# Kernel optimization log

Measured on AMD Instinct MI355X. Metric: run time of the kernel, lower is better.

## Reference

```python
import jax, jax.numpy as jnp
import numpy as np
import math

WINDOW = 257
W = (WINDOW - 1) // 2      # 128
Q_CH = WINDOW + 1          # 258 (query chunk size / stride)
K_CH = WINDOW * 2          # 514 (key window size)


def compl_mod(m, n):
    return int(n * math.ceil(m / n) - m)


def setup_inputs() -> dict:
    key = jax.random.key(0)
    k1, k2, k3 = jax.random.split(key, 3)
    b, s, nh, h = 2, 4096, 16, 64
    q = jax.random.normal(k1, (b, s, nh, h), jnp.float32)
    k = jax.random.normal(k2, (b, s, nh, h), jnp.float32)
    v = jax.random.normal(k3, (b, s, nh, h), jnp.float32)
    return {"q": q, "k": k, "v": v}


def reference(q, k, v):
    b, s, nh, h = q.shape
    q = q * h ** (-0.5)
    q_pad = compl_mod(s, Q_CH)
    k_pad = compl_mod(s + 2 * W - K_CH, Q_CH)
    c = (s + q_pad) // Q_CH  # number of chunks

    # pad along sequence dim (q right-padded; k/v haloed by w on both sides)
    qp = jnp.pad(q, ((0, 0), (0, q_pad), (0, 0), (0, 0)))
    kp = jnp.pad(k, ((0, 0), (W, W + k_pad), (0, 0), (0, 0)))
    vp = jnp.pad(v, ((0, 0), (W, W + k_pad), (0, 0), (0, 0)))

    # unfold: q non-overlapping chunks, k/v overlapping windows (size K_CH, stride Q_CH)
    qw = qp.reshape(b, c, Q_CH, nh, h)                              # [b,c,q,nh,h]
    idx = (jnp.arange(c) * Q_CH)[:, None] + jnp.arange(K_CH)[None]  # [c,K_CH]
    kw = kp[:, idx]                                                 # [b,c,k,nh,h]
    vw = vp[:, idx]

    A = jnp.einsum('bcqnh,bcknh->bncqk', qw, kw)  # [b,nh,c,Q_CH,K_CH]

    # banded mask: valid iff i <= j <= i + 2w (True = masked)
    i = jnp.arange(Q_CH)[:, None]
    j = jnp.arange(K_CH)[None, :]
    base = ~((j >= i) & (j <= i + 2 * W))
    mask_left = base.at[:, :W].set(True)                    # first chunk: no left halo
    mask_right = base.at[:, K_CH - (W + k_pad):].set(True)  # last chunk: no right halo/pad
    if c > 1:
        mask = jnp.concatenate(
            [mask_left[None], jnp.broadcast_to(base, (c - 2, Q_CH, K_CH)), mask_right[None]], axis=0)
    else:
        mask = (mask_left | mask_right)[None]

    mask_value = -jnp.finfo(A.dtype).max
    A = jnp.where(mask[None, None], mask_value, A)
    A = jax.nn.softmax(A, axis=-1)  # dropout omitted (eval mode)

    z = jnp.einsum('bncqk,bcknh->bncqh', A, vw)       # [b,nh,c,Q_CH,h]
    z = z.reshape(b, nh, c * Q_CH, h)[:, :, :s]       # trim q padding
    return jnp.transpose(z, (0, 2, 1, 3))             # [b,s,nh,h]
```

## Files before the change

### kernel.cpp

```cpp
#include <hip/hip_runtime.h>

typedef _Float16 h16;
typedef __attribute__((ext_vector_type(2))) _Float16 f16x2;
typedef __attribute__((ext_vector_type(4))) _Float16 f16x4;
typedef __attribute__((ext_vector_type(2))) __fp16   fp16x2n;
typedef __attribute__((ext_vector_type(8))) _Float16 f16x8;
typedef __attribute__((ext_vector_type(4))) float f32x4;

#define S_LEN 4096
#define NHEAD 16
#define HDIM  64
#define WIN   128
#define TQ    128
#define NCHT  12
#define KSTR  72
#define VSTR2 40
#define SSTR  40
#define QSCALE 0.18033688011112042f

static __device__ __forceinline__ f16x2 pk(float a, float b) {
    fp16x2n r = __builtin_amdgcn_cvt_pkrtz(a, b);
    return __builtin_bit_cast(f16x2, r);
}

static __device__ __forceinline__ f16x8 cvt8(float4 a, float4 b) {
    f16x2 p0 = pk(a.x, a.y), p1 = pk(a.z, a.w);
    f16x2 p2 = pk(b.x, b.y), p3 = pk(b.z, b.w);
    f16x8 r;
    r[0]=p0[0]; r[1]=p0[1]; r[2]=p1[0]; r[3]=p1[1];
    r[4]=p2[0]; r[5]=p2[1]; r[6]=p3[0]; r[7]=p3[1];
    return r;
}

__global__ __launch_bounds__(512, 4)
void wattn(const float* __restrict__ Qg, const float* __restrict__ Kg,
           const float* __restrict__ Vg, float* __restrict__ Og)
{
    __shared__ h16 Kbuf[3][32 * KSTR];
    __shared__ h16 Vbuf[3][64 * VSTR2];
    __shared__ h16 Slds[8 * 16 * SSTR];

    const int tid  = threadIdx.x;
    const int wid  = tid >> 6;
    const int lane = tid & 63;
    const int l15  = lane & 15;
    const int quad = lane >> 4;

    const int q0    = blockIdx.x * TQ;
    const int head  = blockIdx.y;
    const int b     = blockIdx.z;
    const int kbase = q0 - WIN;
    const int rowstride = NHEAD * HDIM;

    const float* KB = Kg + ((long)b * S_LEN * NHEAD + head) * HDIM;
    const float* VB = Vg + ((long)b * S_LEN * NHEAD + head) * HDIM;

    const int srow = tid >> 4;
    const int sh0  = (tid & 15) * 4;

    float4 kreg, vreg;
    #define SLOAD(i) do {                                                    \
        int kg_ = kbase + (i)*32 + srow;                                     \
        kg_ = kg_ < 0 ? 0 : (kg_ > S_LEN-1 ? S_LEN-1 : kg_);                 \
        const float* kp_ = KB + (long)kg_ * rowstride + sh0;                 \
        const float* vp_ = VB + (long)kg_ * rowstride + sh0;                 \
        kreg = *(const float4*)kp_;                                          \
        vreg = *(const float4*)vp_;                                          \
    } while (0)
    #define SWRITE(i) do {                                                   \
        int bi_ = (i) % 3;                                                   \
        f16x2 ka_ = pk(kreg.x, kreg.y), kb_ = pk(kreg.z, kreg.w);            \
        f16x4 kv_; kv_[0]=ka_[0]; kv_[1]=ka_[1]; kv_[2]=kb_[0]; kv_[3]=kb_[1];\
        *(f16x4*)&Kbuf[bi_][srow * KSTR + sh0] = kv_;                        \
        Vbuf[bi_][(sh0+0) * VSTR2 + srow] = (h16)vreg.x;                     \
        Vbuf[bi_][(sh0+1) * VSTR2 + srow] = (h16)vreg.y;                     \
        Vbuf[bi_][(sh0+2) * VSTR2 + srow] = (h16)vreg.z;                     \
        Vbuf[bi_][(sh0+3) * VSTR2 + srow] = (h16)vreg.w;                     \
    } while (0)

    SLOAD(0);

    f16x8 aQ0, aQ1;
    {
        const int qrow = q0 + wid * 16 + l15;
        const float* qp = Qg + ((long)(b * S_LEN + qrow) * NHEAD + head) * HDIM;
        float4 x0 = *(const float4*)(qp + quad*8);
        float4 x1 = *(const float4*)(qp + quad*8 + 4);
        float4 x2 = *(const float4*)(qp + 32 + quad*8);
        float4 x3 = *(const float4*)(qp + 32 + quad*8 + 4);
        x0.x*=QSCALE; x0.y*=QSCALE; x0.z*=QSCALE; x0.w*=QSCALE;
        x1.x*=QSCALE; x1.y*=QSCALE; x1.z*=QSCALE; x1.w*=QSCALE;
        x2.x*=QSCALE; x2.y*=QSCALE; x2.z*=QSCALE; x2.w*=QSCALE;
        x3.x*=QSCALE; x3.y*=QSCALE; x3.z*=QSCALE; x3.w*=QSCALE;
        aQ0 = cvt8(x0, x1);
        aQ1 = cvt8(x2, x3);
    }

    SWRITE(0);
    __syncthreads();

    int lo[4], hi[4];
    #pragma unroll
    for (int r = 0; r < 4; ++r) {
        int qg = q0 + wid*16 + quad*4 + r;
        lo[r] = (qg - WIN < 0) ? 0 : qg - WIN;
        hi[r] = (qg + WIN > S_LEN-1) ? S_LEN-1 : qg + WIN;
    }

    float l_r[4] = {0.f, 0.f, 0.f, 0.f};
    f32x4 Oacc[4];
    #pragma unroll
    for (int t = 0; t < 4; ++t) Oacc[t] = (f32x4){0.f,0.f,0.f,0.f};

    const int c0 = wid >> 1;
    h16* Sw = &Slds[wid * 16 * SSTR];

    for (int i = 0; i < NCHT; ++i) {
        if (i + 1 < NCHT) SLOAD(i + 1);

        if ((unsigned)(i - c0) < 9u) {
            const h16* Kb = Kbuf[i % 3];
            const h16* Vb = Vbuf[i % 3];

            f16x8 bK00 = *(const f16x8*)&Kb[ l15      * KSTR + quad*8];
            f16x8 bK01 = *(const f16x8*)&Kb[ l15      * KSTR + 32 + quad*8];
            f16x8 bK10 = *(const f16x8*)&Kb[(16+l15)  * KSTR + quad*8];
            f16x8 bK11 = *(const f16x8*)&Kb[(16+l15)  * KSTR + 32 + quad*8];

            f32x4 s0 = (f32x4){0.f,0.f,0.f,0.f};
            s0 = __builtin_amdgcn_mfma_f32_16x16x32_f16(aQ0, bK00, s0, 0, 0, 0);
            s0 = __builtin_amdgcn_mfma_f32_16x16x32_f16(aQ1, bK01, s0, 0, 0, 0);
            f32x4 s1 = (f32x4){0.f,0.f,0.f,0.f};
            s1 = __builtin_amdgcn_mfma_f32_16x16x32_f16(aQ0, bK10, s1, 0, 0, 0);
            s1 = __builtin_amdgcn_mfma_f32_16x16x32_f16(aQ1, bK11, s1, 0, 0, 0);

            const int col0 = kbase + i*32 + l15;
            const int col1 = col0 + 16;
            #pragma unroll
            for (int r = 0; r < 4; ++r) {
                float v0 = (col0 >= lo[r] && col0 <= hi[r]) ? s0[r] : -1e30f;
                float v1 = (col1 >= lo[r] && col1 <= hi[r]) ? s1[r] : -1e30f;
                float p0 = exp2f(v0);
                float p1 = exp2f(v1);
                l_r[r] += p0 + p1;
                Sw[(quad*4 + r) * SSTR + l15]      = (h16)p0;
                Sw[(quad*4 + r) * SSTR + 16 + l15] = (h16)p1;
            }

            __builtin_amdgcn_wave_barrier();

            f16x8 aP = *(const f16x8*)&Sw[l15 * SSTR + quad * 8];
            #pragma unroll
            for (int t = 0; t < 4; ++t) {
                f16x8 bV = *(const f16x8*)&Vb[(t*16 + l15) * VSTR2 + quad*8];
                Oacc[t] = __builtin_amdgcn_mfma_f32_16x16x32_f16(aP, bV, Oacc[t], 0, 0, 0);
            }
            __builtin_amdgcn_wave_barrier();
        }

        if (i + 1 < NCHT) SWRITE(i + 1);
        __syncthreads();
    }
    #undef SLOAD
    #undef SWRITE

    float* op = Og + ((long)(b * S_LEN + q0 + wid*16) * NHEAD + head) * HDIM;
    #pragma unroll
    for (int r = 0; r < 4; ++r) {
        float l = l_r[r];
        l += __shfl_xor(l, 1);
        l += __shfl_xor(l, 2);
        l += __shfl_xor(l, 4);
        l += __shfl_xor(l, 8);
        float inv = 1.0f / l;
        #pragma unroll
        for (int t = 0; t < 4; ++t) {
            op[(quad*4 + r) * rowstride + t*16 + l15] = Oacc[t][r] * inv;
        }
    }
}

extern "C" void kernel_launch(void* const* d_in, const int* in_sizes, int n_in,
                              void* d_out, int out_size, void* d_ws, size_t ws_size,
                              hipStream_t stream) {
    const float* q = (const float*)d_in[0];
    const float* k = (const float*)d_in[1];
    const float* v = (const float*)d_in[2];
    float* out = (float*)d_out;
    const int batch = in_sizes[0] / (S_LEN * NHEAD * HDIM);
    dim3 grid(S_LEN / TQ, NHEAD, batch);
    wattn<<<grid, 512, 0, stream>>>(q, k, v, out);
}
```

Before: 155.1 us.

## Double query tile to 256 with 16 waves, split K/V staging, swizzle LDS and blocks

Each block now covers 256 queries with 1024 threads (16 waves), so each staged K/V window is shared by twice as many queries and halo reloads drop. Staging is split: half the threads load K and half load V, one float4 each. XOR swizzles on the transposed V writes and on the P scratch reads and writes are meant to cut LDS bank conflicts. A block-index swizzle remaps workgroups across XCDs for L2 locality. The cost is a block barrier across 16 waves per chunk, and the 4-blocks-per-CU occupancy hint becomes 8 with 1024 threads, which is unlikely to be met.

```diff
diff --git a/kernel.cpp b/kernel.cpp
--- a/kernel.cpp
+++ b/kernel.cpp
@@ -11,8 +11,9 @@
 #define NHEAD 16
 #define HDIM  64
 #define WIN   128
-#define TQ    128
-#define NCHT  12
+#define TQ    256
+#define NQT   (S_LEN / TQ)
+#define NCHT  16
 #define KSTR  72
 #define VSTR2 40
 #define SSTR  40
@@ -32,13 +33,13 @@
     return r;
 }
 
-__global__ __launch_bounds__(512, 4)
+__global__ __launch_bounds__(1024, 8)
 void wattn(const float* __restrict__ Qg, const float* __restrict__ Kg,
            const float* __restrict__ Vg, float* __restrict__ Og)
 {
     __shared__ h16 Kbuf[3][32 * KSTR];
     __shared__ h16 Vbuf[3][64 * VSTR2];
-    __shared__ h16 Slds[8 * 16 * SSTR];
+    __shared__ h16 Slds[16 * 16 * SSTR];
 
     const int tid  = threadIdx.x;
     const int wid  = tid >> 6;
@@ -46,36 +47,45 @@
     const int l15  = lane & 15;
     const int quad = lane >> 4;
 
-    const int q0    = blockIdx.x * TQ;
-    const int head  = blockIdx.y;
-    const int b     = blockIdx.z;
+    int lin = blockIdx.x + NQT * (blockIdx.y + NHEAD * blockIdx.z);
+    int nwg = NQT * NHEAD * gridDim.z;
+    int swz = ((nwg & 7) == 0) ? ((lin & 7) * (nwg >> 3) + (lin >> 3)) : lin;
+    const int bx   = swz & (NQT - 1);
+    const int head = (swz / NQT) & (NHEAD - 1);
+    const int b    = swz / (NQT * NHEAD);
+
+    const int q0    = bx * TQ;
     const int kbase = q0 - WIN;
     const int rowstride = NHEAD * HDIM;
 
     const float* KB = Kg + ((long)b * S_LEN * NHEAD + head) * HDIM;
     const float* VB = Vg + ((long)b * S_LEN * NHEAD + head) * HDIM;
 
-    const int srow = tid >> 4;
-    const int sh0  = (tid & 15) * 4;
-
-    float4 kreg, vreg;
+    const bool isK = (tid < 512);
+    const int srow = (tid >> 4) & 31;
+    const int ish  = tid & 15;
+    const int sh0  = ish * 4;
+    const int vkey = ((srow + (((ish >> 2) & 3) << 3)) & 31) ^ ((ish & 3) << 3);
+    const float* SB = isK ? KB : VB;
+
+    float4 sreg;
     #define SLOAD(i) do {                                                    \
         int kg_ = kbase + (i)*32 + srow;                                     \
         kg_ = kg_ < 0 ? 0 : (kg_ > S_LEN-1 ? S_LEN-1 : kg_);                 \
-        const float* kp_ = KB + (long)kg_ * rowstride + sh0;                 \
-        const float* vp_ = VB + (long)kg_ * rowstride + sh0;                 \
-        kreg = *(const float4*)kp_;                                          \
-        vreg = *(const float4*)vp_;                                          \
+        sreg = *(const float4*)(SB + (long)kg_ * rowstride + sh0);           \
     } while (0)
     #define SWRITE(i) do {                                                   \
         int bi_ = (i) % 3;                                                   \
-        f16x2 ka_ = pk(kreg.x, kreg.y), kb_ = pk(kreg.z, kreg.w);            \
-        f16x4 kv_; kv_[0]=ka_[0]; kv_[1]=ka_[1]; kv_[2]=kb_[0]; kv_[3]=kb_[1];\
-        *(f16x4*)&Kbuf[bi_][srow * KSTR + sh0] = kv_;                        \
-        Vbuf[bi_][(sh0+0) * VSTR2 + srow] = (h16)vreg.x;                     \
-        Vbuf[bi_][(sh0+1) * VSTR2 + srow] = (h16)vreg.y;                     \
-        Vbuf[bi_][(sh0+2) * VSTR2 + srow] = (h16)vreg.z;                     \
-        Vbuf[bi_][(sh0+3) * VSTR2 + srow] = (h16)vreg.w;                     \
+        if (isK) {                                                           \
+            f16x2 ka_ = pk(sreg.x, sreg.y), kb_ = pk(sreg.z, sreg.w);        \
+            f16x4 kv_; kv_[0]=ka_[0]; kv_[1]=ka_[1]; kv_[2]=kb_[0]; kv_[3]=kb_[1];\
+            *(f16x4*)&Kbuf[bi_][srow * KSTR + sh0] = kv_;                    \
+        } else {                                                             \
+            Vbuf[bi_][(sh0+0) * VSTR2 + vkey] = (h16)sreg.x;                 \
+            Vbuf[bi_][(sh0+1) * VSTR2 + vkey] = (h16)sreg.y;                 \
+            Vbuf[bi_][(sh0+2) * VSTR2 + vkey] = (h16)sreg.z;                 \
+            Vbuf[bi_][(sh0+3) * VSTR2 + vkey] = (h16)sreg.w;                 \
+        }                                                                    \
     } while (0)
 
     SLOAD(0);
@@ -114,6 +124,8 @@
 
     const int c0 = wid >> 1;
     h16* Sw = &Slds[wid * 16 * SSTR];
+    const int pxw = quad << 3;
+    const int pxr = (l15 & 12) << 1;
 
     for (int i = 0; i < NCHT; ++i) {
         if (i + 1 < NCHT) SLOAD(i + 1);
@@ -143,16 +155,17 @@
                 float p0 = exp2f(v0);
                 float p1 = exp2f(v1);
                 l_r[r] += p0 + p1;
-                Sw[(quad*4 + r) * SSTR + l15]      = (h16)p0;
-                Sw[(quad*4 + r) * SSTR + 16 + l15] = (h16)p1;
+                Sw[(quad*4 + r) * SSTR + ( l15       ^ pxw)] = (h16)p0;
+                Sw[(quad*4 + r) * SSTR + ((16 + l15) ^ pxw)] = (h16)p1;
             }
 
             __builtin_amdgcn_wave_barrier();
 
-            f16x8 aP = *(const f16x8*)&Sw[l15 * SSTR + quad * 8];
+            f16x8 aP = *(const f16x8*)&Sw[l15 * SSTR + ((quad*8) ^ pxr)];
             #pragma unroll
             for (int t = 0; t < 4; ++t) {
-                f16x8 bV = *(const f16x8*)&Vb[(t*16 + l15) * VSTR2 + quad*8];
+                f16x8 bV = *(const f16x8*)&Vb[(t*16 + l15) * VSTR2 +
+                                              (((quad*8 + (t << 3)) & 31) ^ pxr)];
                 Oacc[t] = __builtin_amdgcn_mfma_f32_16x16x32_f16(aP, bV, Oacc[t], 0, 0, 0);
             }
             __builtin_amdgcn_wave_barrier();
@@ -188,6 +201,6 @@
     const float* v = (const float*)d_in[2];
     float* out = (float*)d_out;
     const int batch = in_sizes[0] / (S_LEN * NHEAD * HDIM);
-    dim3 grid(S_LEN / TQ, NHEAD, batch);
-    wattn<<<grid, 512, 0, stream>>>(q, k, v, out);
-}
+    dim3 grid(NQT, NHEAD, batch);
+    wattn<<<grid, 1024, 0, stream>>>(q, k, v, out);
+}
```

Result: slower. 208.7 us (+34.5%).
